# Kernel tuning notes

Measured on AMD Instinct MI355X. Metric: run time of the kernel, lower is better.

## Reference

```python
import jax, jax.numpy as jnp
import numpy as np

BS, DEC, IN_LEN, HID, EMB, VOCAB = 16, 100, 512, 768, 768, 32000


def setup_inputs() -> dict:
    key = jax.random.key(0)
    ks = jax.random.split(key, 8)
    x = jax.random.normal(ks[0], (BS, DEC, HID), dtype=jnp.float32)
    attn_dist = jax.random.normal(ks[1], (BS, DEC, IN_LEN), dtype=jnp.float32)
    enc_input = jax.random.randint(ks[2], (BS, IN_LEN), 0, VOCAB, dtype=jnp.int32)
    enc_output = jax.random.normal(ks[3], (BS, IN_LEN, EMB), dtype=jnp.float32)
    # learned params
    W_vocab = jax.random.normal(ks[4], (HID, VOCAB), dtype=jnp.float32) / np.sqrt(HID)
    b_vocab = jnp.zeros((VOCAB,), dtype=jnp.float32)
    W_gen = jax.random.normal(ks[5], (HID + EMB, 1), dtype=jnp.float32) / np.sqrt(HID + EMB)
    b_gen = jnp.zeros((1,), dtype=jnp.float32)
    return {"x": x, "attn_dist": attn_dist, "enc_input": enc_input,
            "enc_output": enc_output, "W_vocab": W_vocab, "b_vocab": b_vocab,
            "W_gen": W_gen, "b_gen": b_gen}


def reference(x, attn_dist, enc_input, enc_output, W_vocab, b_vocab, W_gen, b_gen):
    # context vector: [bs, dec, emb] = attn @ enc_output
    context = jnp.einsum('bdl,ble->bde', attn_dist, enc_output)
    mix = jnp.concatenate([context, x], axis=2)              # [bs, dec, emb+hid]
    p_gen = jax.nn.sigmoid(mix @ W_gen + b_gen)              # [bs, dec, 1]
    logit = x @ W_vocab + b_vocab                            # [bs, dec, vocab]
    vocab_dist = jax.nn.softmax(logit, axis=2) * p_gen       # [bs, dec, vocab]
    attn_w = jax.nn.softmax(attn_dist, axis=2) * (1.0 - p_gen)  # [bs, dec, in_len]
    # scatter_add attention mass onto vocab ids (duplicate ids accumulate)
    b_idx = jnp.arange(BS)[:, None, None]
    d_idx = jnp.arange(DEC)[None, :, None]
    v_idx = enc_input[:, None, :]                            # broadcast over dec
    mixed = vocab_dist.at[b_idx, d_idx, v_idx].add(attn_w)
    return jnp.log(mixed)
```

## Files before the change

### kernel.cpp

```cpp
#include <hip/hip_runtime.h>
#include <math.h>

#define BS 16
#define DEC 100
#define IN_LEN 512
#define HID 768
#define EMB 768
#define VOCAB 32000
#define NROW (BS*DEC)
#define NTILE_M 13
#define NTILE_N 250
#define KT 12
#define TILE_SHORTS 8192

using short8 = __attribute__((ext_vector_type(8))) short;
using ushort4v = __attribute__((ext_vector_type(4))) unsigned short;
using f32x4 = __attribute__((ext_vector_type(4))) float;

__device__ __forceinline__ unsigned short f2bf(float f) {
  unsigned u = __float_as_uint(f);
  u = u + 0x7FFFu + ((u >> 16) & 1u);
  return (unsigned short)(u >> 16);
}
__device__ __forceinline__ float bf2f(unsigned short h) {
  return __uint_as_float(((unsigned)h) << 16);
}

__device__ __forceinline__ void gll16(const void* g, void* l) {
  __builtin_amdgcn_global_load_lds(
      (const __attribute__((address_space(1))) unsigned int*)g,
      (__attribute__((address_space(3))) unsigned int*)l, 16, 0, 0);
}

__global__ __launch_bounds__(256) void k0_venc(const float* __restrict__ enc_out,
                                               const float* __restrict__ Wg,
                                               float* __restrict__ venc) {
  int row = blockIdx.x * 4 + (threadIdx.x >> 6);
  int lane = threadIdx.x & 63;
  const float* p = enc_out + (size_t)row * EMB;
  float s = 0.f;
  for (int e = lane; e < EMB; e += 64) s += p[e] * Wg[e];
  for (int off = 32; off; off >>= 1) s += __shfl_xor(s, off);
  if (lane == 0) venc[row] = s;
}

__global__ __launch_bounds__(256) void k1_row(const float* __restrict__ attn,
                                              const float* __restrict__ x,
                                              const float* __restrict__ venc,
                                              const float* __restrict__ Wg,
                                              const float* __restrict__ bgen,
                                              float* __restrict__ pg,
                                              float* __restrict__ lp,
                                              float* __restrict__ m_a,
                                              float* __restrict__ s_a) {
  int r = blockIdx.x;
  int b = r / DEC;
  int tid = threadIdx.x;
  const float* arow = attn + (size_t)r * IN_LEN;
  const float* ve = venc + b * IN_LEN;
  const float* xrow = x + (size_t)r * HID;

  float pdot = 0.f, m = -1e30f;
  for (int l = tid; l < IN_LEN; l += 256) { float a = arow[l]; pdot += a * ve[l]; m = fmaxf(m, a); }
  for (int h = tid; h < HID; h += 256) pdot += xrow[h] * Wg[HID + h];

  for (int off = 32; off; off >>= 1) pdot += __shfl_xor(pdot, off);
  for (int off = 32; off; off >>= 1) m = fmaxf(m, __shfl_xor(m, off));

  __shared__ float red[8];
  if ((tid & 63) == 0) { red[tid >> 6] = pdot; red[4 + (tid >> 6)] = m; }
  __syncthreads();
  float z = red[0] + red[1] + red[2] + red[3];
  m = fmaxf(fmaxf(red[4], red[5]), fmaxf(red[6], red[7]));

  float se = 0.f;
  for (int l = tid; l < IN_LEN; l += 256) se += expf(arow[l] - m);
  for (int off = 32; off; off >>= 1) se += __shfl_xor(se, off);
  __syncthreads();
  if ((tid & 63) == 0) red[tid >> 6] = se;
  __syncthreads();
  se = red[0] + red[1] + red[2] + red[3];

  if (tid == 0) {
    z += bgen[0];
    float p, l_p;
    if (z >= 0.f) { float e = expf(-z); p = 1.f / (1.f + e); l_p = -log1pf(e); }
    else          { float e = expf(z);  p = e / (1.f + e);   l_p = z - log1pf(e); }
    pg[r] = p; lp[r] = l_p; m_a[r] = m; s_a[r] = se;
  }
}

__global__ __launch_bounds__(256) void p0_pack_x(const float* __restrict__ X,
                                                 unsigned short* __restrict__ Xp) {
  int mtile = blockIdx.x, kt = blockIdx.y, tid = threadIdx.x;
  size_t base = ((size_t)(mtile * KT + kt)) * TILE_SHORTS;
#pragma unroll
  for (int i = 0; i < 4; i++) {
    int slot = tid + i * 256;
    int r = slot >> 3, s = slot & 7;
    int row = mtile * 128 + r;
    int k0 = kt * 64 + ((s ^ (r & 7)) << 3);
    short8 v;
    if (row < NROW) {
      const float* p = X + (size_t)row * HID + k0;
#pragma unroll
      for (int j = 0; j < 8; j++) v[j] = (short)f2bf(p[j]);
    } else {
#pragma unroll
      for (int j = 0; j < 8; j++) v[j] = 0;
    }
    *(short8*)&Xp[base + (size_t)slot * 8] = v;
  }
}

__global__ __launch_bounds__(256) void p0_pack_w(const float* __restrict__ W,
                                                 unsigned short* __restrict__ Wp) {
  __shared__ float ld[64][129];
  int ntile = blockIdx.x, kt = blockIdx.y, tid = threadIdx.x;
#pragma unroll
  for (int i = 0; i < 32; i++) {
    int idx = tid + i * 256;
    int kk = idx >> 7, nn = idx & 127;
    ld[kk][nn] = W[(size_t)(kt * 64 + kk) * VOCAB + ntile * 128 + nn];
  }
  __syncthreads();
  size_t base = ((size_t)(ntile * KT + kt)) * TILE_SHORTS;
#pragma unroll
  for (int i = 0; i < 4; i++) {
    int slot = tid + i * 256;
    int n = slot >> 3, s = slot & 7;
    int k0 = (s ^ (n & 7)) << 3;
    short8 v;
#pragma unroll
    for (int j = 0; j < 8; j++) v[j] = (short)f2bf(ld[k0 + j][n]);
    *(short8*)&Wp[base + (size_t)slot * 8] = v;
  }
}

__global__ __launch_bounds__(256) void k2_gemm_bf16(const unsigned short* __restrict__ Xp,
                                                    const unsigned short* __restrict__ Wp,
                                                    const float* __restrict__ bvocab,
                                                    float* __restrict__ out,
                                                    unsigned short* __restrict__ lbf,
                                                    float* __restrict__ part,
                                                    int use_bf) {
  __shared__ __align__(16) unsigned short sh[2][2][TILE_SHORTS];

  int bid = blockIdx.x;
  const int NWG = NTILE_M * NTILE_N;
  const int q = NWG / 8, rr = NWG % 8;
  int xcd = bid & 7, idx = bid >> 3;
  int wg = (xcd < rr ? xcd * (q + 1) : rr * (q + 1) + (xcd - rr) * q) + idx;
  int ntile = wg / NTILE_M, mtile = wg % NTILE_M;

  int tid = threadIdx.x;
  int wid = tid >> 6, lane = tid & 63;
  int wr = wid >> 1, wc = wid & 1;
  int l15 = lane & 15, hi = lane >> 4;

  const unsigned short* aSrc = Xp + (size_t)(mtile * KT) * TILE_SHORTS;
  const unsigned short* bSrc = Wp + (size_t)(ntile * KT) * TILE_SHORTS;

  f32x4 acc[4][4] = {};

#pragma unroll
  for (int j = 0; j < 4; j++) {
    gll16(aSrc + (size_t)(tid + j * 256) * 8, &sh[0][0][(tid + j * 256) * 8]);
    gll16(bSrc + (size_t)(tid + j * 256) * 8, &sh[0][1][(tid + j * 256) * 8]);
  }
  __syncthreads();

  int buf = 0;
  for (int kt = 0; kt < KT; kt++) {
    if (kt + 1 < KT) {
      const unsigned short* a = aSrc + (size_t)(kt + 1) * TILE_SHORTS;
      const unsigned short* b = bSrc + (size_t)(kt + 1) * TILE_SHORTS;
      int nb = buf ^ 1;
#pragma unroll
      for (int j = 0; j < 4; j++) {
        gll16(a + (size_t)(tid + j * 256) * 8, &sh[nb][0][(tid + j * 256) * 8]);
        gll16(b + (size_t)(tid + j * 256) * 8, &sh[nb][1][(tid + j * 256) * 8]);
      }
    }
    const unsigned short* A = &sh[buf][0][0];
    const unsigned short* B = &sh[buf][1][0];
#pragma unroll
    for (int ksub = 0; ksub < 2; ksub++) {
      short8 af[4], bfr[4];
#pragma unroll
      for (int mm = 0; mm < 4; mm++) {
        int r = wr * 64 + mm * 16 + l15;
        int phys = (ksub * 4 + hi) ^ (r & 7);
        af[mm] = *(const short8*)&A[r * 64 + phys * 8];
      }
#pragma unroll
      for (int nn = 0; nn < 4; nn++) {
        int n = wc * 64 + nn * 16 + l15;
        int phys = (ksub * 4 + hi) ^ (n & 7);
        bfr[nn] = *(const short8*)&B[n * 64 + phys * 8];
      }
#pragma unroll
      for (int mm = 0; mm < 4; mm++)
#pragma unroll
        for (int nn = 0; nn < 4; nn++)
          acc[mm][nn] = __builtin_amdgcn_mfma_f32_16x16x32_bf16(af[mm], bfr[nn], acc[mm][nn], 0, 0, 0);
    }
    __syncthreads();
    buf ^= 1;
  }

  float bb[4];
#pragma unroll
  for (int nn = 0; nn < 4; nn++) bb[nn] = bvocab[ntile * 128 + wc * 64 + nn * 16 + l15];
#pragma unroll
  for (int mm = 0; mm < 4; mm++)
#pragma unroll
    for (int nn = 0; nn < 4; nn++)
#pragma unroll
      for (int j = 0; j < 4; j++) acc[mm][nn][j] += bb[nn];

  float* ldsC = (float*)sh;
#pragma unroll
  for (int mm = 0; mm < 4; mm++) {
    int r0 = wr * 64 + mm * 16 + hi * 4;
#pragma unroll
    for (int nn = 0; nn < 4; nn++) {
      int c = wc * 64 + nn * 16 + l15;
#pragma unroll
      for (int j = 0; j < 4; j++) ldsC[(r0 + j) * 128 + c] = acc[mm][nn][j];
    }
  }
  __syncthreads();

  if (use_bf) {
#pragma unroll
    for (int i = 0; i < 8; i++) {
      int flat = tid + i * 256;
      int r = flat >> 4, c = (flat & 15) * 8;
      int grow = mtile * 128 + r;
      if (grow < NROW) {
        const float* p = &ldsC[r * 128 + c];
        short8 v;
#pragma unroll
        for (int j = 0; j < 8; j++) v[j] = (short)f2bf(p[j]);
        *(short8*)&lbf[(size_t)grow * VOCAB + ntile * 128 + c] = v;
      }
    }
  } else {
#pragma unroll
    for (int i = 0; i < 16; i++) {
      int flat = tid + i * 256;
      int r = flat >> 5, c = (flat & 31) * 4;
      int grow = mtile * 128 + r;
      if (grow < NROW)
        *(float4*)&out[(size_t)grow * VOCAB + ntile * 128 + c] = *(const float4*)&ldsC[r * 128 + c];
    }
  }
  __syncthreads();

  float* red = (float*)sh;
#pragma unroll
  for (int mm = 0; mm < 4; mm++) {
#pragma unroll
    for (int j = 0; j < 4; j++) {
      float mx = fmaxf(fmaxf(acc[mm][0][j], acc[mm][1][j]),
                       fmaxf(acc[mm][2][j], acc[mm][3][j]));
      mx = fmaxf(mx, __shfl_xor(mx, 1));
      mx = fmaxf(mx, __shfl_xor(mx, 2));
      mx = fmaxf(mx, __shfl_xor(mx, 4));
      mx = fmaxf(mx, __shfl_xor(mx, 8));
      float sl = __expf(acc[mm][0][j] - mx) + __expf(acc[mm][1][j] - mx) +
                 __expf(acc[mm][2][j] - mx) + __expf(acc[mm][3][j] - mx);
      sl += __shfl_xor(sl, 1);
      sl += __shfl_xor(sl, 2);
      sl += __shfl_xor(sl, 4);
      sl += __shfl_xor(sl, 8);
      if (l15 == 0) {
        int rloc = wr * 64 + mm * 16 + hi * 4 + j;
        int o = (rloc * 2 + wc) * 2;
        red[o] = mx; red[o + 1] = sl;
      }
    }
  }
  __syncthreads();
  if (tid < 128) {
    int o0 = (tid * 2 + 0) * 2;
    int o1 = (tid * 2 + 1) * 2;
    float m0 = red[o0], s0 = red[o0 + 1];
    float m1 = red[o1], s1 = red[o1 + 1];
    float m = fmaxf(m0, m1);
    float s = s0 * __expf(m0 - m) + s1 * __expf(m1 - m);
    int grow = mtile * 128 + tid;
    if (grow < NROW) {
      part[(size_t)grow * 500 + ntile * 2]     = m;
      part[(size_t)grow * 500 + ntile * 2 + 1] = s;
    }
  }
}

__global__ __launch_bounds__(256) void k4_finish(float* __restrict__ out,
                                                 const float* __restrict__ part,
                                                 const float* __restrict__ lp) {
  int r = blockIdx.x >> 1, half = blockIdx.x & 1;
  int tid = threadIdx.x;
  float m = -1e30f, s = 0.f;
  if (tid < NTILE_N) {
    m = part[(size_t)r * 500 + tid * 2];
    s = part[(size_t)r * 500 + tid * 2 + 1];
  }
  for (int off = 1; off < 64; off <<= 1) {
    float mo = __shfl_xor(m, off), so = __shfl_xor(s, off);
    float nm = fmaxf(m, mo);
    s = s * __expf(m - nm) + so * __expf(mo - nm);
    m = nm;
  }
  __shared__ float sm[4], ss[4], sc[1];
  if ((tid & 63) == 0) { sm[tid >> 6] = m; ss[tid >> 6] = s; }
  __syncthreads();
  if (tid == 0) {
    float mm_ = sm[0], ss_ = ss[0];
    for (int w = 1; w < 4; w++) {
      float nm = fmaxf(mm_, sm[w]);
      ss_ = ss_ * __expf(mm_ - nm) + ss[w] * __expf(sm[w] - nm);
      mm_ = nm;
    }
    sc[0] = lp[r] - (mm_ + __logf(ss_));
  }
  __syncthreads();
  float coef = sc[0];
  float4* p = (float4*)(out + (size_t)r * VOCAB + half * (VOCAB / 2));
  for (int i = tid; i < VOCAB / 8; i += 256) {
    float4 v = p[i];
    v.x += coef; v.y += coef; v.z += coef; v.w += coef;
    p[i] = v;
  }
}

__global__ __launch_bounds__(256) void k4_finish_bf(float* __restrict__ out,
                                                    const unsigned short* __restrict__ lbf,
                                                    const float* __restrict__ part,
                                                    const float* __restrict__ lp) {
  int r = blockIdx.x;
  int tid = threadIdx.x;
  float m = -1e30f, s = 0.f;
  if (tid < NTILE_N) {
    m = part[(size_t)r * 500 + tid * 2];
    s = part[(size_t)r * 500 + tid * 2 + 1];
  }
  for (int off = 1; off < 64; off <<= 1) {
    float mo = __shfl_xor(m, off), so = __shfl_xor(s, off);
    float nm = fmaxf(m, mo);
    s = s * __expf(m - nm) + so * __expf(mo - nm);
    m = nm;
  }
  __shared__ float sm[4], ss[4], sc[1];
  if ((tid & 63) == 0) { sm[tid >> 6] = m; ss[tid >> 6] = s; }
  __syncthreads();
  if (tid == 0) {
    float mm_ = sm[0], ss_ = ss[0];
    for (int w = 1; w < 4; w++) {
      float nm = fmaxf(mm_, sm[w]);
      ss_ = ss_ * __expf(mm_ - nm) + ss[w] * __expf(sm[w] - nm);
      mm_ = nm;
    }
    sc[0] = lp[r] - (mm_ + __logf(ss_));
  }
  __syncthreads();
  float coef = sc[0];
  const short8* src = (const short8*)(lbf + (size_t)r * VOCAB);
  float* dst = out + (size_t)r * VOCAB;
  for (int i = tid; i < VOCAB / 8; i += 256) {
    short8 v = src[i];
    float4 a, b;
    a.x = bf2f((unsigned short)v[0]) + coef; a.y = bf2f((unsigned short)v[1]) + coef;
    a.z = bf2f((unsigned short)v[2]) + coef; a.w = bf2f((unsigned short)v[3]) + coef;
    b.x = bf2f((unsigned short)v[4]) + coef; b.y = bf2f((unsigned short)v[5]) + coef;
    b.z = bf2f((unsigned short)v[6]) + coef; b.w = bf2f((unsigned short)v[7]) + coef;
    *(float4*)&dst[i * 8]     = a;
    *(float4*)&dst[i * 8 + 4] = b;
  }
}

__global__ __launch_bounds__(256) void k4_scatter(float* __restrict__ out,
                                                  const float* __restrict__ attn,
                                                  const int* __restrict__ enc,
                                                  const float* __restrict__ pg,
                                                  const float* __restrict__ m_a,
                                                  const float* __restrict__ s_a) {
  int idx = blockIdx.x * 256 + threadIdx.x;
  int l = idx & (IN_LEN - 1);
  int r = idx >> 9;
  int b = r / DEC;
  float omp = 1.f - pg[r];
  if (omp <= 0.f) return;
  float term = omp * expf(attn[(size_t)r * IN_LEN + l] - m_a[r]) / s_a[r];
  int v = enc[b * IN_LEN + l];
  unsigned* ua = (unsigned*)(out + (size_t)r * VOCAB + v);
  unsigned old = *ua;
  while (true) {
    float f = __uint_as_float(old);
    float nf = logf(expf(f) + term);
    unsigned assumed = old;
    old = atomicCAS(ua, assumed, __float_as_uint(nf));
    if (old == assumed) break;
  }
}

#define BM 128
#define BN 128
#define BK 32
__device__ __forceinline__ int swz_old(int row, int k) {
  int slot = (k >> 3) ^ ((row >> 1) & 3);
  return row * 32 + slot * 8 + (k & 7);
}

__global__ __launch_bounds__(256) void k2_gemm_old(const float* __restrict__ X,
                                                   const float* __restrict__ W,
                                                   const float* __restrict__ bvocab,
                                                   float* __restrict__ out) {
  __shared__ __align__(16) unsigned short As[BM * BK];
  __shared__ __align__(16) unsigned short Bs[BN * BK];
  const int mtile = blockIdx.x;
  const int ntile = blockIdx.y;
  const int tid = threadIdx.x;
  const int wid = tid >> 6, lane = tid & 63;
  const int wr = wid >> 1, wc = wid & 1;
  f32x4 acc[4][4] = {};
  float4 areg[4];
  float  breg[16];
  const int nl = tid & 127;
  const int kg = tid >> 7;
  {
#pragma unroll
    for (int i = 0; i < 4; i++) {
      int idx = tid + i * 256;
      int r = mtile * BM + (idx >> 3);
      if (r < NROW) areg[i] = *(const float4*)(X + (size_t)r * HID + (idx & 7) * 4);
      else areg[i] = make_float4(0.f, 0.f, 0.f, 0.f);
    }
    const float* base = W + (size_t)(kg * 16) * VOCAB + ntile * BN + nl;
#pragma unroll
    for (int i = 0; i < 16; i++) breg[i] = base[(size_t)i * VOCAB];
  }
  const int KS = HID / BK;
  for (int ks = 0; ks < KS; ++ks) {
#pragma unroll
    for (int i = 0; i < 4; i++) {
      int idx = tid + i * 256;
      int r = idx >> 3, kq = idx & 7;
      ushort4v w;
      w[0] = f2bf(areg[i].x); w[1] = f2bf(areg[i].y);
      w[2] = f2bf(areg[i].z); w[3] = f2bf(areg[i].w);
      *(ushort4v*)&As[swz_old(r, kq * 4)] = w;
    }
    {
      short8 v0, v1;
#pragma unroll
      for (int i = 0; i < 8; i++) { v0[i] = (short)f2bf(breg[i]); v1[i] = (short)f2bf(breg[8 + i]); }
      *(short8*)&Bs[swz_old(nl, kg * 16)] = v0;
      *(short8*)&Bs[swz_old(nl, kg * 16 + 8)] = v1;
    }
    __syncthreads();
    if (ks + 1 < KS) {
      const int ksn = ks + 1;
#pragma unroll
      for (int i = 0; i < 4; i++) {
        int idx = tid + i * 256;
        int r = mtile * BM + (idx >> 3);
        if (r < NROW) areg[i] = *(const float4*)(X + (size_t)r * HID + ksn * BK + (idx & 7) * 4);
        else areg[i] = make_float4(0.f, 0.f, 0.f, 0.f);
      }
      const float* base = W + (size_t)(ksn * BK + kg * 16) * VOCAB + ntile * BN + nl;
#pragma unroll
      for (int i = 0; i < 16; i++) breg[i] = base[(size_t)i * VOCAB];
    }
    {
      const int k0 = (lane >> 4) * 8;
      const int rbase = wr * 64 + (lane & 15);
      const int cbase = wc * 64 + (lane & 15);
      short8 af[4], bf[4];
#pragma unroll
      for (int mm = 0; mm < 4; mm++) af[mm] = *(const short8*)&As[swz_old(rbase + mm * 16, k0)];
#pragma unroll
      for (int nn = 0; nn < 4; nn++) bf[nn] = *(const short8*)&Bs[swz_old(cbase + nn * 16, k0)];
#pragma unroll
      for (int mm = 0; mm < 4; mm++)
#pragma unroll
        for (int nn = 0; nn < 4; nn++)
          acc[mm][nn] = __builtin_amdgcn_mfma_f32_16x16x32_bf16(af[mm], bf[nn], acc[mm][nn], 0, 0, 0);
    }
    __syncthreads();
  }
#pragma unroll
  for (int mm = 0; mm < 4; mm++) {
    int row0 = mtile * BM + wr * 64 + mm * 16 + (lane >> 4) * 4;
#pragma unroll
    for (int nn = 0; nn < 4; nn++) {
      int col = ntile * BN + wc * 64 + nn * 16 + (lane & 15);
      float bb = bvocab[col];
#pragma unroll
      for (int j = 0; j < 4; j++) {
        int row = row0 + j;
        if (row < NROW) out[(size_t)row * VOCAB + col] = acc[mm][nn][j] + bb;
      }
    }
  }
}

__global__ __launch_bounds__(256) void k3_norm(float* __restrict__ out,
                                               const float* __restrict__ lp) {
  int r = blockIdx.x;
  float4* row = reinterpret_cast<float4*>(out + (size_t)r * VOCAB);
  int tid = threadIdx.x;
  float m = -1e30f, s = 0.f;
  for (int i = tid; i < VOCAB / 4; i += 256) {
    float4 v = row[i];
    float m4 = fmaxf(fmaxf(v.x, v.y), fmaxf(v.z, v.w));
    if (m4 > m) { s *= __expf(m - m4); m = m4; }
    s += __expf(v.x - m) + __expf(v.y - m) + __expf(v.z - m) + __expf(v.w - m);
  }
  for (int off = 32; off; off >>= 1) {
    float mo = __shfl_xor(m, off), so = __shfl_xor(s, off);
    float nm = fmaxf(m, mo);
    s = s * __expf(m - nm) + so * __expf(mo - nm);
    m = nm;
  }
  __shared__ float mred[4], sred[4];
  if ((tid & 63) == 0) { mred[tid >> 6] = m; sred[tid >> 6] = s; }
  __syncthreads();
  if (tid == 0) {
    float mm = mred[0], ss = sred[0];
    for (int w = 1; w < 4; w++) {
      float mo = mred[w], so = sred[w];
      float nm = fmaxf(mm, mo);
      ss = ss * __expf(mm - nm) + so * __expf(mo - nm);
      mm = nm;
    }
    mred[0] = mm; sred[0] = ss;
  }
  __syncthreads();
  m = mred[0]; s = sred[0];
  float coef = lp[r] - (m + __logf(s));
  for (int i = tid; i < VOCAB / 4; i += 256) {
    float4 v = row[i];
    v.x += coef; v.y += coef; v.z += coef; v.w += coef;
    row[i] = v;
  }
}

extern "C" void kernel_launch(void* const* d_in, const int* in_sizes, int n_in,
                              void* d_out, int out_size, void* d_ws, size_t ws_size,
                              hipStream_t stream) {
  (void)in_sizes; (void)n_in; (void)out_size;
  const float* x       = (const float*)d_in[0];
  const float* attn    = (const float*)d_in[1];
  const int*   enc_in  = (const int*)d_in[2];
  const float* enc_out = (const float*)d_in[3];
  const float* Wv      = (const float*)d_in[4];
  const float* bv      = (const float*)d_in[5];
  const float* Wg      = (const float*)d_in[6];
  const float* bg      = (const float*)d_in[7];
  float* out = (float*)d_out;
  float* ws  = (float*)d_ws;

  float* venc = ws;
  float* pg   = ws + 8192;
  float* lp   = ws + 9792;
  float* m_a  = ws + 11392;
  float* s_a  = ws + 12992;
  float* part = ws + 14592;
  unsigned short* Xp = (unsigned short*)(ws + 814592);
  unsigned short* Wp = (unsigned short*)(ws + 1453568);
  unsigned short* Lbf = (unsigned short*)(ws + 13741568);
  const size_t NEED  = (size_t)13741568 * 4;
  const size_t NEED2 = NEED + (size_t)NROW * VOCAB * 2;

  hipLaunchKernelGGL(k0_venc, dim3(2048), dim3(256), 0, stream, enc_out, Wg, venc);
  hipLaunchKernelGGL(k1_row, dim3(NROW), dim3(256), 0, stream, attn, x, venc, Wg, bg,
                     pg, lp, m_a, s_a);

  if (ws_size >= NEED) {
    int use_bf = (ws_size >= NEED2) ? 1 : 0;
    hipLaunchKernelGGL(p0_pack_x, dim3(NTILE_M, KT), dim3(256), 0, stream, x, Xp);
    hipLaunchKernelGGL(p0_pack_w, dim3(NTILE_N, KT), dim3(256), 0, stream, Wv, Wp);
    hipLaunchKernelGGL(k2_gemm_bf16, dim3(NTILE_M * NTILE_N), dim3(256), 0, stream,
                       Xp, Wp, bv, out, Lbf, part, use_bf);
    if (use_bf) {
      hipLaunchKernelGGL(k4_finish_bf, dim3(NROW), dim3(256), 0, stream, out, Lbf, part, lp);
    } else {
      hipLaunchKernelGGL(k4_finish, dim3(NROW * 2), dim3(256), 0, stream, out, part, lp);
    }
    hipLaunchKernelGGL(k4_scatter, dim3((NROW * IN_LEN) / 256), dim3(256), 0, stream,
                       out, attn, enc_in, pg, m_a, s_a);
  } else {
    hipLaunchKernelGGL(k2_gemm_old, dim3(NTILE_M, NTILE_N), dim3(256), 0, stream,
                       x, Wv, bv, out);
    hipLaunchKernelGGL(k3_norm, dim3(NROW), dim3(256), 0, stream, out, lp);
    hipLaunchKernelGGL(k4_scatter, dim3((NROW * IN_LEN) / 256), dim3(256), 0, stream,
                       out, attn, enc_in, pg, m_a, s_a);
  }
}
```

Measured before the change: 293.8 us.

## Widen GEMM tile to 128x256 with triple-buffered K32 pipeline and bf16 LDS epilogue

The vocab GEMM now uses 128x256 output tiles and K-steps of 32 instead of 128x128 and 64. It loads through a three-stage LDS ring with explicit vmcnt waits so two stages of loads are in flight, and raises MFMA priority with setprio. The epilogue writes bf16 values into LDS and copies them out with wide stores, and the partial softmax stats are resized. The finish kernel uses 512 threads. The aim is more reuse of each A/B tile, fewer workgroups and better overlap of loads with compute, at the cost of more accumulator registers (32 f32x4) and possible occupancy limits.

```diff
diff --git a/kernel.cpp b/kernel.cpp
--- a/kernel.cpp
+++ b/kernel.cpp
@@ -9,9 +9,10 @@
 #define VOCAB 32000
 #define NROW (BS*DEC)
 #define NTILE_M 13
-#define NTILE_N 250
-#define KT 12
-#define TILE_SHORTS 8192
+#define NTILE_N2 125
+#define KT2 24
+#define A_SHORTS 4096
+#define B_SHORTS 8192
 
 using short8 = __attribute__((ext_vector_type(8))) short;
 using ushort4v = __attribute__((ext_vector_type(4))) unsigned short;
@@ -92,14 +93,14 @@
 
 __global__ __launch_bounds__(256) void p0_pack_x(const float* __restrict__ X,
                                                  unsigned short* __restrict__ Xp) {
-  int mtile = blockIdx.x, kt = blockIdx.y, tid = threadIdx.x;
-  size_t base = ((size_t)(mtile * KT + kt)) * TILE_SHORTS;
-#pragma unroll
-  for (int i = 0; i < 4; i++) {
+  int mtile = blockIdx.x, ks = blockIdx.y, tid = threadIdx.x;
+  size_t base = ((size_t)(mtile * KT2 + ks)) * A_SHORTS;
+#pragma unroll
+  for (int i = 0; i < 2; i++) {
     int slot = tid + i * 256;
-    int r = slot >> 3, s = slot & 7;
+    int r = slot >> 2, s = slot & 3;
     int row = mtile * 128 + r;
-    int k0 = kt * 64 + ((s ^ (r & 7)) << 3);
+    int k0 = ks * 32 + ((s ^ (r & 3)) << 3);
     short8 v;
     if (row < NROW) {
       const float* p = X + (size_t)row * HID + k0;
@@ -115,21 +116,21 @@
 
 __global__ __launch_bounds__(256) void p0_pack_w(const float* __restrict__ W,
                                                  unsigned short* __restrict__ Wp) {
-  __shared__ float ld[64][129];
-  int ntile = blockIdx.x, kt = blockIdx.y, tid = threadIdx.x;
+  __shared__ float ld[32][257];
+  int ntile = blockIdx.x, ks = blockIdx.y, tid = threadIdx.x;
 #pragma unroll
   for (int i = 0; i < 32; i++) {
     int idx = tid + i * 256;
-    int kk = idx >> 7, nn = idx & 127;
-    ld[kk][nn] = W[(size_t)(kt * 64 + kk) * VOCAB + ntile * 128 + nn];
-  }
-  __syncthreads();
-  size_t base = ((size_t)(ntile * KT + kt)) * TILE_SHORTS;
+    int kk = idx >> 8, nn = idx & 255;
+    ld[kk][nn] = W[(size_t)(ks * 32 + kk) * VOCAB + ntile * 256 + nn];
+  }
+  __syncthreads();
+  size_t base = ((size_t)(ntile * KT2 + ks)) * B_SHORTS;
 #pragma unroll
   for (int i = 0; i < 4; i++) {
     int slot = tid + i * 256;
-    int n = slot >> 3, s = slot & 7;
-    int k0 = (s ^ (n & 7)) << 3;
+    int n = slot >> 2, s = slot & 3;
+    int k0 = (s ^ (n & 3)) << 3;
     short8 v;
 #pragma unroll
     for (int j = 0; j < 8; j++) v[j] = (short)f2bf(ld[k0 + j][n]);
@@ -137,140 +138,143 @@
   }
 }
 
-__global__ __launch_bounds__(256) void k2_gemm_bf16(const unsigned short* __restrict__ Xp,
-                                                    const unsigned short* __restrict__ Wp,
-                                                    const float* __restrict__ bvocab,
-                                                    float* __restrict__ out,
-                                                    unsigned short* __restrict__ lbf,
-                                                    float* __restrict__ part,
-                                                    int use_bf) {
-  __shared__ __align__(16) unsigned short sh[2][2][TILE_SHORTS];
+__global__ __launch_bounds__(256, 2) void k2_gemm_v4(const unsigned short* __restrict__ Xp,
+                                                     const unsigned short* __restrict__ Wp,
+                                                     const float* __restrict__ bvocab,
+                                                     float* __restrict__ out,
+                                                     unsigned short* __restrict__ lbf,
+                                                     float* __restrict__ part,
+                                                     int use_bf) {
+  __shared__ __align__(16) unsigned short sh[3][12288];
 
   int bid = blockIdx.x;
-  const int NWG = NTILE_M * NTILE_N;
+  const int NWG = NTILE_M * NTILE_N2;
   const int q = NWG / 8, rr = NWG % 8;
   int xcd = bid & 7, idx = bid >> 3;
   int wg = (xcd < rr ? xcd * (q + 1) : rr * (q + 1) + (xcd - rr) * q) + idx;
   int ntile = wg / NTILE_M, mtile = wg % NTILE_M;
 
-  int tid = threadIdx.x;
-  int wid = tid >> 6, lane = tid & 63;
-  int wr = wid >> 1, wc = wid & 1;
-  int l15 = lane & 15, hi = lane >> 4;
-
-  const unsigned short* aSrc = Xp + (size_t)(mtile * KT) * TILE_SHORTS;
-  const unsigned short* bSrc = Wp + (size_t)(ntile * KT) * TILE_SHORTS;
-
-  f32x4 acc[4][4] = {};
-
-#pragma unroll
-  for (int j = 0; j < 4; j++) {
-    gll16(aSrc + (size_t)(tid + j * 256) * 8, &sh[0][0][(tid + j * 256) * 8]);
-    gll16(bSrc + (size_t)(tid + j * 256) * 8, &sh[0][1][(tid + j * 256) * 8]);
-  }
-  __syncthreads();
-
-  int buf = 0;
-  for (int kt = 0; kt < KT; kt++) {
-    if (kt + 1 < KT) {
-      const unsigned short* a = aSrc + (size_t)(kt + 1) * TILE_SHORTS;
-      const unsigned short* b = bSrc + (size_t)(kt + 1) * TILE_SHORTS;
-      int nb = buf ^ 1;
-#pragma unroll
-      for (int j = 0; j < 4; j++) {
-        gll16(a + (size_t)(tid + j * 256) * 8, &sh[nb][0][(tid + j * 256) * 8]);
-        gll16(b + (size_t)(tid + j * 256) * 8, &sh[nb][1][(tid + j * 256) * 8]);
+  const int tid = threadIdx.x;
+  const int wid = tid >> 6, lane = tid & 63;
+  const int wr = wid >> 1, wc = wid & 1;
+  const int l15 = lane & 15, hi = lane >> 4;
+  const int phys = (hi ^ (l15 & 3)) * 8;
+
+  const unsigned short* aSrc = Xp + (size_t)(mtile * KT2) * A_SHORTS;
+  const unsigned short* bSrc = Wp + (size_t)(ntile * KT2) * B_SHORTS;
+
+  const int aoff = (wr * 64 + l15) * 32 + phys;
+  const int boff = (wc * 128 + l15) * 32 + phys;
+
+  f32x4 acc[4][8] = {};
+
+#pragma unroll
+  for (int t = 0; t < 2; t++) {
+    const unsigned short* a = aSrc + (size_t)t * A_SHORTS;
+    const unsigned short* b = bSrc + (size_t)t * B_SHORTS;
+    unsigned short* dA = &sh[t][0];
+    unsigned short* dB = &sh[t][4096];
+    gll16(a + (size_t)tid * 8,            dA + tid * 8);
+    gll16(a + (size_t)(tid + 256) * 8,    dA + (tid + 256) * 8);
+#pragma unroll
+    for (int j2 = 0; j2 < 4; j2++)
+      gll16(b + (size_t)(tid + j2 * 256) * 8, dB + (tid + j2 * 256) * 8);
+  }
+  asm volatile("s_waitcnt vmcnt(6)" ::: "memory");
+  __builtin_amdgcn_s_barrier();
+  asm volatile("" ::: "memory");
+
+  int bcur = 0;
+  for (int t = 0; t < KT2; ++t) {
+    if (t + 2 < KT2) {
+      int bn = bcur + 2; if (bn >= 3) bn -= 3;
+      const unsigned short* a = aSrc + (size_t)(t + 2) * A_SHORTS;
+      const unsigned short* b = bSrc + (size_t)(t + 2) * B_SHORTS;
+      unsigned short* dA = &sh[bn][0];
+      unsigned short* dB = &sh[bn][4096];
+      gll16(a + (size_t)tid * 8,            dA + tid * 8);
+      gll16(a + (size_t)(tid + 256) * 8,    dA + (tid + 256) * 8);
+#pragma unroll
+      for (int j2 = 0; j2 < 4; j2++)
+        gll16(b + (size_t)(tid + j2 * 256) * 8, dB + (tid + j2 * 256) * 8);
+    }
+    const unsigned short* A = &sh[bcur][0];
+    const unsigned short* B = &sh[bcur][4096];
+    short8 af[4], bfr[8];
+#pragma unroll
+    for (int mm = 0; mm < 4; mm++) af[mm] = *(const short8*)&A[aoff + mm * 512];
+#pragma unroll
+    for (int nn = 0; nn < 8; nn++) bfr[nn] = *(const short8*)&B[boff + nn * 512];
+    __builtin_amdgcn_s_setprio(1);
+#pragma unroll
+    for (int mm = 0; mm < 4; mm++)
+#pragma unroll
+      for (int nn = 0; nn < 8; nn++)
+        acc[mm][nn] = __builtin_amdgcn_mfma_f32_16x16x32_bf16(af[mm], bfr[nn], acc[mm][nn], 0, 0, 0);
+    __builtin_amdgcn_s_setprio(0);
+    if (t < KT2 - 2) { asm volatile("s_waitcnt vmcnt(6)" ::: "memory"); }
+    else             { asm volatile("s_waitcnt vmcnt(0)" ::: "memory"); }
+    __builtin_amdgcn_s_barrier();
+    asm volatile("" ::: "memory");
+    bcur = bcur + 1; if (bcur >= 3) bcur = 0;
+  }
+
+  __syncthreads();
+
+  float bb[8];
+#pragma unroll
+  for (int nn = 0; nn < 8; nn++) bb[nn] = bvocab[ntile * 256 + wc * 128 + nn * 16 + l15];
+#pragma unroll
+  for (int mm = 0; mm < 4; mm++)
+#pragma unroll
+    for (int nn = 0; nn < 8; nn++)
+#pragma unroll
+      for (int j = 0; j < 4; j++) acc[mm][nn][j] += bb[nn];
+
+  unsigned short* ldsC = &sh[0][0];
+  float* red = (float*)&sh[2][8192];
+
+  if (use_bf) {
+#pragma unroll
+    for (int mm = 0; mm < 4; mm++) {
+      int row0 = wr * 64 + mm * 16 + hi * 4;
+#pragma unroll
+      for (int nn = 0; nn < 8; nn++) {
+        int col = wc * 128 + nn * 16 + l15;
+#pragma unroll
+        for (int j = 0; j < 4; j++) ldsC[(row0 + j) * 256 + col] = f2bf(acc[mm][nn][j]);
       }
     }
-    const unsigned short* A = &sh[buf][0][0];
-    const unsigned short* B = &sh[buf][1][0];
-#pragma unroll
-    for (int ksub = 0; ksub < 2; ksub++) {
-      short8 af[4], bfr[4];
-#pragma unroll
-      for (int mm = 0; mm < 4; mm++) {
-        int r = wr * 64 + mm * 16 + l15;
-        int phys = (ksub * 4 + hi) ^ (r & 7);
-        af[mm] = *(const short8*)&A[r * 64 + phys * 8];
+  } else {
+#pragma unroll
+    for (int mm = 0; mm < 4; mm++) {
+      int row0 = mtile * 128 + wr * 64 + mm * 16 + hi * 4;
+#pragma unroll
+      for (int nn = 0; nn < 8; nn++) {
+        int col = ntile * 256 + wc * 128 + nn * 16 + l15;
+#pragma unroll
+        for (int j = 0; j < 4; j++) {
+          int row = row0 + j;
+          if (row < NROW) out[(size_t)row * VOCAB + col] = acc[mm][nn][j];
+        }
       }
-#pragma unroll
-      for (int nn = 0; nn < 4; nn++) {
-        int n = wc * 64 + nn * 16 + l15;
-        int phys = (ksub * 4 + hi) ^ (n & 7);
-        bfr[nn] = *(const short8*)&B[n * 64 + phys * 8];
-      }
-#pragma unroll
-      for (int mm = 0; mm < 4; mm++)
-#pragma unroll
-        for (int nn = 0; nn < 4; nn++)
-          acc[mm][nn] = __builtin_amdgcn_mfma_f32_16x16x32_bf16(af[mm], bfr[nn], acc[mm][nn], 0, 0, 0);
-    }
-    __syncthreads();
-    buf ^= 1;
-  }
-
-  float bb[4];
-#pragma unroll
-  for (int nn = 0; nn < 4; nn++) bb[nn] = bvocab[ntile * 128 + wc * 64 + nn * 16 + l15];
-#pragma unroll
-  for (int mm = 0; mm < 4; mm++)
-#pragma unroll
-    for (int nn = 0; nn < 4; nn++)
-#pragma unroll
-      for (int j = 0; j < 4; j++) acc[mm][nn][j] += bb[nn];
-
-  float* ldsC = (float*)sh;
+    }
+  }
+
 #pragma unroll
   for (int mm = 0; mm < 4; mm++) {
-    int r0 = wr * 64 + mm * 16 + hi * 4;
-#pragma unroll
-    for (int nn = 0; nn < 4; nn++) {
-      int c = wc * 64 + nn * 16 + l15;
-#pragma unroll
-      for (int j = 0; j < 4; j++) ldsC[(r0 + j) * 128 + c] = acc[mm][nn][j];
-    }
-  }
-  __syncthreads();
-
-  if (use_bf) {
-#pragma unroll
-    for (int i = 0; i < 8; i++) {
-      int flat = tid + i * 256;
-      int r = flat >> 4, c = (flat & 15) * 8;
-      int grow = mtile * 128 + r;
-      if (grow < NROW) {
-        const float* p = &ldsC[r * 128 + c];
-        short8 v;
-#pragma unroll
-        for (int j = 0; j < 8; j++) v[j] = (short)f2bf(p[j]);
-        *(short8*)&lbf[(size_t)grow * VOCAB + ntile * 128 + c] = v;
-      }
-    }
-  } else {
-#pragma unroll
-    for (int i = 0; i < 16; i++) {
-      int flat = tid + i * 256;
-      int r = flat >> 5, c = (flat & 31) * 4;
-      int grow = mtile * 128 + r;
-      if (grow < NROW)
-        *(float4*)&out[(size_t)grow * VOCAB + ntile * 128 + c] = *(const float4*)&ldsC[r * 128 + c];
-    }
-  }
-  __syncthreads();
-
-  float* red = (float*)sh;
-#pragma unroll
-  for (int mm = 0; mm < 4; mm++) {
 #pragma unroll
     for (int j = 0; j < 4; j++) {
-      float mx = fmaxf(fmaxf(acc[mm][0][j], acc[mm][1][j]),
-                       fmaxf(acc[mm][2][j], acc[mm][3][j]));
+      float mx = acc[mm][0][j];
+#pragma unroll
+      for (int nn = 1; nn < 8; nn++) mx = fmaxf(mx, acc[mm][nn][j]);
       mx = fmaxf(mx, __shfl_xor(mx, 1));
       mx = fmaxf(mx, __shfl_xor(mx, 2));
       mx = fmaxf(mx, __shfl_xor(mx, 4));
       mx = fmaxf(mx, __shfl_xor(mx, 8));
-      float sl = __expf(acc[mm][0][j] - mx) + __expf(acc[mm][1][j] - mx) +
-                 __expf(acc[mm][2][j] - mx) + __expf(acc[mm][3][j] - mx);
+      float sl = 0.f;
+#pragma unroll
+      for (int nn = 0; nn < 8; nn++) sl += __expf(acc[mm][nn][j] - mx);
       sl += __shfl_xor(sl, 1);
       sl += __shfl_xor(sl, 2);
       sl += __shfl_xor(sl, 4);
@@ -283,6 +287,17 @@
     }
   }
   __syncthreads();
+
+  if (use_bf) {
+#pragma unroll
+    for (int i = 0; i < 16; i++) {
+      int flat = tid + i * 256;
+      int r = flat >> 5, c = (flat & 31) * 8;
+      int grow = mtile * 128 + r;
+      if (grow < NROW)
+        *(short8*)&lbf[(size_t)grow * VOCAB + ntile * 256 + c] = *(const short8*)&ldsC[r * 256 + c];
+    }
+  }
   if (tid < 128) {
     int o0 = (tid * 2 + 0) * 2;
     int o1 = (tid * 2 + 1) * 2;
@@ -292,60 +307,22 @@
     float s = s0 * __expf(m0 - m) + s1 * __expf(m1 - m);
     int grow = mtile * 128 + tid;
     if (grow < NROW) {
-      part[(size_t)grow * 500 + ntile * 2]     = m;
-      part[(size_t)grow * 500 + ntile * 2 + 1] = s;
-    }
-  }
-}
-
-__global__ __launch_bounds__(256) void k4_finish(float* __restrict__ out,
-                                                 const float* __restrict__ part,
-                                                 const float* __restrict__ lp) {
-  int r = blockIdx.x >> 1, half = blockIdx.x & 1;
-  int tid = threadIdx.x;
-  float m = -1e30f, s = 0.f;
-  if (tid < NTILE_N) {
-    m = part[(size_t)r * 500 + tid * 2];
-    s = part[(size_t)r * 500 + tid * 2 + 1];
-  }
-  for (int off = 1; off < 64; off <<= 1) {
-    float mo = __shfl_xor(m, off), so = __shfl_xor(s, off);
-    float nm = fmaxf(m, mo);
-    s = s * __expf(m - nm) + so * __expf(mo - nm);
-    m = nm;
-  }
-  __shared__ float sm[4], ss[4], sc[1];
-  if ((tid & 63) == 0) { sm[tid >> 6] = m; ss[tid >> 6] = s; }
-  __syncthreads();
-  if (tid == 0) {
-    float mm_ = sm[0], ss_ = ss[0];
-    for (int w = 1; w < 4; w++) {
-      float nm = fmaxf(mm_, sm[w]);
-      ss_ = ss_ * __expf(mm_ - nm) + ss[w] * __expf(sm[w] - nm);
-      mm_ = nm;
-    }
-    sc[0] = lp[r] - (mm_ + __logf(ss_));
-  }
-  __syncthreads();
-  float coef = sc[0];
-  float4* p = (float4*)(out + (size_t)r * VOCAB + half * (VOCAB / 2));
-  for (int i = tid; i < VOCAB / 8; i += 256) {
-    float4 v = p[i];
-    v.x += coef; v.y += coef; v.z += coef; v.w += coef;
-    p[i] = v;
-  }
-}
-
-__global__ __launch_bounds__(256) void k4_finish_bf(float* __restrict__ out,
+      part[(size_t)grow * 256 + ntile * 2]     = m;
+      part[(size_t)grow * 256 + ntile * 2 + 1] = s;
+    }
+  }
+}
+
+__global__ __launch_bounds__(512) void k4_finish_bf(float* __restrict__ out,
                                                     const unsigned short* __restrict__ lbf,
                                                     const float* __restrict__ part,
                                                     const float* __restrict__ lp) {
   int r = blockIdx.x;
   int tid = threadIdx.x;
   float m = -1e30f, s = 0.f;
-  if (tid < NTILE_N) {
-    m = part[(size_t)r * 500 + tid * 2];
-    s = part[(size_t)r * 500 + tid * 2 + 1];
+  if (tid < NTILE_N2) {
+    m = part[(size_t)r * 256 + tid * 2];
+    s = part[(size_t)r * 256 + tid * 2 + 1];
   }
   for (int off = 1; off < 64; off <<= 1) {
     float mo = __shfl_xor(m, off), so = __shfl_xor(s, off);
@@ -353,12 +330,12 @@
     s = s * __expf(m - nm) + so * __expf(mo - nm);
     m = nm;
   }
-  __shared__ float sm[4], ss[4], sc[1];
+  __shared__ float sm[8], ss[8], sc[1];
   if ((tid & 63) == 0) { sm[tid >> 6] = m; ss[tid >> 6] = s; }
   __syncthreads();
   if (tid == 0) {
     float mm_ = sm[0], ss_ = ss[0];
-    for (int w = 1; w < 4; w++) {
+    for (int w = 1; w < 8; w++) {
       float nm = fmaxf(mm_, sm[w]);
       ss_ = ss_ * __expf(mm_ - nm) + ss[w] * __expf(sm[w] - nm);
       mm_ = nm;
@@ -369,7 +346,7 @@
   float coef = sc[0];
   const short8* src = (const short8*)(lbf + (size_t)r * VOCAB);
   float* dst = out + (size_t)r * VOCAB;
-  for (int i = tid; i < VOCAB / 8; i += 256) {
+  for (int i = tid; i < VOCAB / 8; i += 512) {
     short8 v = src[i];
     float4 a, b;
     a.x = bf2f((unsigned short)v[0]) + coef; a.y = bf2f((unsigned short)v[1]) + coef;
@@ -378,6 +355,44 @@
     b.z = bf2f((unsigned short)v[6]) + coef; b.w = bf2f((unsigned short)v[7]) + coef;
     *(float4*)&dst[i * 8]     = a;
     *(float4*)&dst[i * 8 + 4] = b;
+  }
+}
+
+__global__ __launch_bounds__(256) void k4_finish(float* __restrict__ out,
+                                                 const float* __restrict__ part,
+                                                 const float* __restrict__ lp) {
+  int r = blockIdx.x >> 1, half = blockIdx.x & 1;
+  int tid = threadIdx.x;
+  float m = -1e30f, s = 0.f;
+  if (tid < NTILE_N2) {
+    m = part[(size_t)r * 256 + tid * 2];
+    s = part[(size_t)r * 256 + tid * 2 + 1];
+  }
+  for (int off = 1; off < 64; off <<= 1) {
+    float mo = __shfl_xor(m, off), so = __shfl_xor(s, off);
+    float nm = fmaxf(m, mo);
+    s = s * __expf(m - nm) + so * __expf(mo - nm);
+    m = nm;
+  }
+  __shared__ float sm[4], ss[4], sc[1];
+  if ((tid & 63) == 0) { sm[tid >> 6] = m; ss[tid >> 6] = s; }
+  __syncthreads();
+  if (tid == 0) {
+    float mm_ = sm[0], ss_ = ss[0];
+    for (int w = 1; w < 4; w++) {
+      float nm = fmaxf(mm_, sm[w]);
+      ss_ = ss_ * __expf(mm_ - nm) + ss[w] * __expf(sm[w] - nm);
+      mm_ = nm;
+    }
+    sc[0] = lp[r] - (mm_ + __logf(ss_));
+  }
+  __syncthreads();
+  float coef = sc[0];
+  float4* p = (float4*)(out + (size_t)r * VOCAB + half * (VOCAB / 2));
+  for (int i = tid; i < VOCAB / 8; i += 256) {
+    float4 v = p[i];
+    v.x += coef; v.y += coef; v.z += coef; v.w += coef;
+    p[i] = v;
   }
 }
 
@@ -581,19 +596,19 @@
 
   if (ws_size >= NEED) {
     int use_bf = (ws_size >= NEED2) ? 1 : 0;
-    hipLaunchKernelGGL(p0_pack_x, dim3(NTILE_M, KT), dim3(256), 0, stream, x, Xp);
-    hipLaunchKernelGGL(p0_pack_w, dim3(NTILE_N, KT), dim3(256), 0, stream, Wv, Wp);
-    hipLaunchKernelGGL(k2_gemm_bf16, dim3(NTILE_M * NTILE_N), dim3(256), 0, stream,
+    hipLaunchKernelGGL(p0_pack_x, dim3(NTILE_M, KT2), dim3(256), 0, stream, x, Xp);
+    hipLaunchKernelGGL(p0_pack_w, dim3(NTILE_N2, KT2), dim3(256), 0, stream, Wv, Wp);
+    hipLaunchKernelGGL(k2_gemm_v4, dim3(NTILE_M * NTILE_N2), dim3(256), 0, stream,
                        Xp, Wp, bv, out, Lbf, part, use_bf);
     if (use_bf) {
-      hipLaunchKernelGGL(k4_finish_bf, dim3(NROW), dim3(256), 0, stream, out, Lbf, part, lp);
+      hipLaunchKernelGGL(k4_finish_bf, dim3(NROW), dim3(512), 0, stream, out, Lbf, part, lp);
     } else {
       hipLaunchKernelGGL(k4_finish, dim3(NROW * 2), dim3(256), 0, stream, out, part, lp);
     }
     hipLaunchKernelGGL(k4_scatter, dim3((NROW * IN_LEN) / 256), dim3(256), 0, stream,
                        out, attn, enc_in, pg, m_a, s_a);
   } else {
-    hipLaunchKernelGGL(k2_gemm_old, dim3(NTILE_M, NTILE_N), dim3(256), 0, stream,
+    hipLaunchKernelGGL(k2_gemm_old, dim3(NTILE_M, 250), dim3(256), 0, stream,
                        x, Wv, bv, out);
     hipLaunchKernelGGL(k3_norm, dim3(NROW), dim3(256), 0, stream, out, lp);
     hipLaunchKernelGGL(k4_scatter, dim3((NROW * IN_LEN) / 256), dim3(256), 0, stream,
```

New measurement: 276.8 us. -5.8%, faster.

## Fuse scatter into finish kernel with LDS hash; single-buffer GEMM LDS staging

Applied to the files above, without the earlier changes.

Merges the log-softmax finish pass and the attention scatter into one per-row kernel. It aggregates duplicate vocab ids in an LDS hash table and then applies log(exp(p)+sum) to the touched entries, which removes a separate kernel and its global atomics. The GEMM drops LDS double buffering so each K step loads and then syncs, which halves LDS use but serialises loads with compute. Its epilogue writes bf16 directly into LDS, and the fp32 path stores straight from registers. The fused update goes through exp and log again, which adds rounding error.

```diff
diff --git a/kernel.cpp b/kernel.cpp
--- a/kernel.cpp
+++ b/kernel.cpp
@@ -11,7 +11,7 @@
 #define NTILE_M 13
 #define NTILE_N 250
 #define KT 12
-#define TILE_SHORTS 8192
+#define T_SHORTS 8192
 
 using short8 = __attribute__((ext_vector_type(8))) short;
 using ushort4v = __attribute__((ext_vector_type(4))) unsigned short;
@@ -93,7 +93,7 @@
 __global__ __launch_bounds__(256) void p0_pack_x(const float* __restrict__ X,
                                                  unsigned short* __restrict__ Xp) {
   int mtile = blockIdx.x, kt = blockIdx.y, tid = threadIdx.x;
-  size_t base = ((size_t)(mtile * KT + kt)) * TILE_SHORTS;
+  size_t base = ((size_t)(mtile * KT + kt)) * T_SHORTS;
 #pragma unroll
   for (int i = 0; i < 4; i++) {
     int slot = tid + i * 256;
@@ -124,7 +124,7 @@
     ld[kk][nn] = W[(size_t)(kt * 64 + kk) * VOCAB + ntile * 128 + nn];
   }
   __syncthreads();
-  size_t base = ((size_t)(ntile * KT + kt)) * TILE_SHORTS;
+  size_t base = ((size_t)(ntile * KT + kt)) * T_SHORTS;
 #pragma unroll
   for (int i = 0; i < 4; i++) {
     int slot = tid + i * 256;
@@ -137,14 +137,15 @@
   }
 }
 
-__global__ __launch_bounds__(256) void k2_gemm_bf16(const unsigned short* __restrict__ Xp,
-                                                    const unsigned short* __restrict__ Wp,
-                                                    const float* __restrict__ bvocab,
-                                                    float* __restrict__ out,
-                                                    unsigned short* __restrict__ lbf,
-                                                    float* __restrict__ part,
-                                                    int use_bf) {
-  __shared__ __align__(16) unsigned short sh[2][2][TILE_SHORTS];
+__global__ __launch_bounds__(256) void k2_gemm_v5(const unsigned short* __restrict__ Xp,
+                                                  const unsigned short* __restrict__ Wp,
+                                                  const float* __restrict__ bvocab,
+                                                  float* __restrict__ out,
+                                                  unsigned short* __restrict__ lbf,
+                                                  float* __restrict__ part,
+                                                  int use_bf) {
+  __shared__ __align__(16) unsigned short sh[2 * T_SHORTS];
+  __shared__ float red[512];
 
   int bid = blockIdx.x;
   const int NWG = NTILE_M * NTILE_N;
@@ -153,37 +154,28 @@
   int wg = (xcd < rr ? xcd * (q + 1) : rr * (q + 1) + (xcd - rr) * q) + idx;
   int ntile = wg / NTILE_M, mtile = wg % NTILE_M;
 
-  int tid = threadIdx.x;
-  int wid = tid >> 6, lane = tid & 63;
-  int wr = wid >> 1, wc = wid & 1;
-  int l15 = lane & 15, hi = lane >> 4;
-
-  const unsigned short* aSrc = Xp + (size_t)(mtile * KT) * TILE_SHORTS;
-  const unsigned short* bSrc = Wp + (size_t)(ntile * KT) * TILE_SHORTS;
+  const int tid = threadIdx.x;
+  const int wid = tid >> 6, lane = tid & 63;
+  const int wr = wid >> 1, wc = wid & 1;
+  const int l15 = lane & 15, hi = lane >> 4;
+
+  const unsigned short* aSrc = Xp + (size_t)(mtile * KT) * T_SHORTS;
+  const unsigned short* bSrc = Wp + (size_t)(ntile * KT) * T_SHORTS;
+  unsigned short* shA = &sh[0];
+  unsigned short* shB = &sh[T_SHORTS];
 
   f32x4 acc[4][4] = {};
 
-#pragma unroll
-  for (int j = 0; j < 4; j++) {
-    gll16(aSrc + (size_t)(tid + j * 256) * 8, &sh[0][0][(tid + j * 256) * 8]);
-    gll16(bSrc + (size_t)(tid + j * 256) * 8, &sh[0][1][(tid + j * 256) * 8]);
-  }
-  __syncthreads();
-
-  int buf = 0;
-  for (int kt = 0; kt < KT; kt++) {
-    if (kt + 1 < KT) {
-      const unsigned short* a = aSrc + (size_t)(kt + 1) * TILE_SHORTS;
-      const unsigned short* b = bSrc + (size_t)(kt + 1) * TILE_SHORTS;
-      int nb = buf ^ 1;
-#pragma unroll
-      for (int j = 0; j < 4; j++) {
-        gll16(a + (size_t)(tid + j * 256) * 8, &sh[nb][0][(tid + j * 256) * 8]);
-        gll16(b + (size_t)(tid + j * 256) * 8, &sh[nb][1][(tid + j * 256) * 8]);
-      }
-    }
-    const unsigned short* A = &sh[buf][0][0];
-    const unsigned short* B = &sh[buf][1][0];
+  for (int kt = 0; kt < KT; ++kt) {
+    const unsigned short* a = aSrc + (size_t)kt * T_SHORTS;
+    const unsigned short* b = bSrc + (size_t)kt * T_SHORTS;
+#pragma unroll
+    for (int p = 0; p < 4; p++) {
+      gll16(a + (size_t)(tid + p * 256) * 8, shA + (tid + p * 256) * 8);
+      gll16(b + (size_t)(tid + p * 256) * 8, shB + (tid + p * 256) * 8);
+    }
+    __syncthreads();
+
 #pragma unroll
     for (int ksub = 0; ksub < 2; ksub++) {
       short8 af[4], bfr[4];
@@ -191,13 +183,13 @@
       for (int mm = 0; mm < 4; mm++) {
         int r = wr * 64 + mm * 16 + l15;
         int phys = (ksub * 4 + hi) ^ (r & 7);
-        af[mm] = *(const short8*)&A[r * 64 + phys * 8];
+        af[mm] = *(const short8*)&shA[r * 64 + phys * 8];
       }
 #pragma unroll
       for (int nn = 0; nn < 4; nn++) {
         int n = wc * 64 + nn * 16 + l15;
         int phys = (ksub * 4 + hi) ^ (n & 7);
-        bfr[nn] = *(const short8*)&B[n * 64 + phys * 8];
+        bfr[nn] = *(const short8*)&shB[n * 64 + phys * 8];
       }
 #pragma unroll
       for (int mm = 0; mm < 4; mm++)
@@ -206,7 +198,6 @@
           acc[mm][nn] = __builtin_amdgcn_mfma_f32_16x16x32_bf16(af[mm], bfr[nn], acc[mm][nn], 0, 0, 0);
     }
     __syncthreads();
-    buf ^= 1;
   }
 
   float bb[4];
@@ -219,46 +210,35 @@
 #pragma unroll
       for (int j = 0; j < 4; j++) acc[mm][nn][j] += bb[nn];
 
-  float* ldsC = (float*)sh;
-#pragma unroll
-  for (int mm = 0; mm < 4; mm++) {
-    int r0 = wr * 64 + mm * 16 + hi * 4;
-#pragma unroll
-    for (int nn = 0; nn < 4; nn++) {
-      int c = wc * 64 + nn * 16 + l15;
-#pragma unroll
-      for (int j = 0; j < 4; j++) ldsC[(r0 + j) * 128 + c] = acc[mm][nn][j];
-    }
-  }
-  __syncthreads();
+  unsigned short* ldsC = &sh[0];
 
   if (use_bf) {
 #pragma unroll
-    for (int i = 0; i < 8; i++) {
-      int flat = tid + i * 256;
-      int r = flat >> 4, c = (flat & 15) * 8;
-      int grow = mtile * 128 + r;
-      if (grow < NROW) {
-        const float* p = &ldsC[r * 128 + c];
-        short8 v;
-#pragma unroll
-        for (int j = 0; j < 8; j++) v[j] = (short)f2bf(p[j]);
-        *(short8*)&lbf[(size_t)grow * VOCAB + ntile * 128 + c] = v;
+    for (int mm = 0; mm < 4; mm++) {
+      int row0 = wr * 64 + mm * 16 + hi * 4;
+#pragma unroll
+      for (int nn = 0; nn < 4; nn++) {
+        int col = wc * 64 + nn * 16 + l15;
+#pragma unroll
+        for (int j = 0; j < 4; j++) ldsC[(row0 + j) * 128 + col] = f2bf(acc[mm][nn][j]);
       }
     }
   } else {
 #pragma unroll
-    for (int i = 0; i < 16; i++) {
-      int flat = tid + i * 256;
-      int r = flat >> 5, c = (flat & 31) * 4;
-      int grow = mtile * 128 + r;
-      if (grow < NROW)
-        *(float4*)&out[(size_t)grow * VOCAB + ntile * 128 + c] = *(const float4*)&ldsC[r * 128 + c];
-    }
-  }
-  __syncthreads();
-
-  float* red = (float*)sh;
+    for (int mm = 0; mm < 4; mm++) {
+      int row0 = mtile * 128 + wr * 64 + mm * 16 + hi * 4;
+#pragma unroll
+      for (int nn = 0; nn < 4; nn++) {
+        int col = ntile * 128 + wc * 64 + nn * 16 + l15;
+#pragma unroll
+        for (int j = 0; j < 4; j++) {
+          int row = row0 + j;
+          if (row < NROW) out[(size_t)row * VOCAB + col] = acc[mm][nn][j];
+        }
+      }
+    }
+  }
+
 #pragma unroll
   for (int mm = 0; mm < 4; mm++) {
 #pragma unroll
@@ -283,6 +263,17 @@
     }
   }
   __syncthreads();
+
+  if (use_bf) {
+#pragma unroll
+    for (int i = 0; i < 8; i++) {
+      int flat = tid + i * 256;
+      int r = flat >> 4, c = (flat & 15) * 8;
+      int grow = mtile * 128 + r;
+      if (grow < NROW)
+        *(short8*)&lbf[(size_t)grow * VOCAB + ntile * 128 + c] = *(const short8*)&ldsC[r * 128 + c];
+    }
+  }
   if (tid < 128) {
     int o0 = (tid * 2 + 0) * 2;
     int o1 = (tid * 2 + 1) * 2;
@@ -298,6 +289,85 @@
   }
 }
 
+__global__ __launch_bounds__(512) void k4_fused(float* __restrict__ out,
+                                                const unsigned short* __restrict__ lbf,
+                                                const float* __restrict__ part,
+                                                const float* __restrict__ lp,
+                                                const float* __restrict__ attn,
+                                                const int* __restrict__ enc,
+                                                const float* __restrict__ pg,
+                                                const float* __restrict__ m_a,
+                                                const float* __restrict__ s_a) {
+  int r = blockIdx.x;
+  int tid = threadIdx.x;
+  __shared__ float sm[8], ss[8], sc[1];
+  __shared__ int   s_key[1024];
+  __shared__ float s_val[1024];
+  s_key[tid] = -1; s_key[tid + 512] = -1;
+  s_val[tid] = 0.f; s_val[tid + 512] = 0.f;
+
+  float m = -1e30f, s = 0.f;
+  if (tid < NTILE_N) {
+    m = part[(size_t)r * 500 + tid * 2];
+    s = part[(size_t)r * 500 + tid * 2 + 1];
+  }
+  for (int off = 1; off < 64; off <<= 1) {
+    float mo = __shfl_xor(m, off), so = __shfl_xor(s, off);
+    float nm = fmaxf(m, mo);
+    s = s * __expf(m - nm) + so * __expf(mo - nm);
+    m = nm;
+  }
+  if ((tid & 63) == 0) { sm[tid >> 6] = m; ss[tid >> 6] = s; }
+  __syncthreads();
+  if (tid == 0) {
+    float mm_ = sm[0], ss_ = ss[0];
+    for (int w = 1; w < 8; w++) {
+      float nm = fmaxf(mm_, sm[w]);
+      ss_ = ss_ * __expf(mm_ - nm) + ss[w] * __expf(sm[w] - nm);
+      mm_ = nm;
+    }
+    sc[0] = lp[r] - (mm_ + __logf(ss_));
+  }
+
+  float omp = 1.f - pg[r];
+  if (omp > 0.f) {
+    int b_ = r / DEC;
+    float t = omp * __expf(attn[(size_t)r * IN_LEN + tid] - m_a[r]) / s_a[r];
+    int v = enc[b_ * IN_LEN + tid];
+    int slot = v & 1023;
+    while (true) {
+      int old = atomicCAS(&s_key[slot], -1, v);
+      if (old == -1 || old == v) { atomicAdd(&s_val[slot], t); break; }
+      slot = (slot + 1) & 1023;
+    }
+  }
+  __syncthreads();
+  float coef = sc[0];
+
+  const short8* src = (const short8*)(lbf + (size_t)r * VOCAB);
+  float* dst = out + (size_t)r * VOCAB;
+  for (int i = tid; i < VOCAB / 8; i += 512) {
+    short8 v = src[i];
+    float4 a, b;
+    a.x = bf2f((unsigned short)v[0]) + coef; a.y = bf2f((unsigned short)v[1]) + coef;
+    a.z = bf2f((unsigned short)v[2]) + coef; a.w = bf2f((unsigned short)v[3]) + coef;
+    b.x = bf2f((unsigned short)v[4]) + coef; b.y = bf2f((unsigned short)v[5]) + coef;
+    b.z = bf2f((unsigned short)v[6]) + coef; b.w = bf2f((unsigned short)v[7]) + coef;
+    *(float4*)&dst[i * 8]     = a;
+    *(float4*)&dst[i * 8 + 4] = b;
+  }
+  __syncthreads();
+
+  for (int i = tid; i < 1024; i += 512) {
+    int v = s_key[i];
+    if (v >= 0) {
+      float sum = s_val[i];
+      float p = dst[v];
+      dst[v] = logf(expf(p) + sum);
+    }
+  }
+}
+
 __global__ __launch_bounds__(256) void k4_finish(float* __restrict__ out,
                                                  const float* __restrict__ part,
                                                  const float* __restrict__ lp) {
@@ -333,51 +403,6 @@
     float4 v = p[i];
     v.x += coef; v.y += coef; v.z += coef; v.w += coef;
     p[i] = v;
-  }
-}
-
-__global__ __launch_bounds__(256) void k4_finish_bf(float* __restrict__ out,
-                                                    const unsigned short* __restrict__ lbf,
-                                                    const float* __restrict__ part,
-                                                    const float* __restrict__ lp) {
-  int r = blockIdx.x;
-  int tid = threadIdx.x;
-  float m = -1e30f, s = 0.f;
-  if (tid < NTILE_N) {
-    m = part[(size_t)r * 500 + tid * 2];
-    s = part[(size_t)r * 500 + tid * 2 + 1];
-  }
-  for (int off = 1; off < 64; off <<= 1) {
-    float mo = __shfl_xor(m, off), so = __shfl_xor(s, off);
-    float nm = fmaxf(m, mo);
-    s = s * __expf(m - nm) + so * __expf(mo - nm);
-    m = nm;
-  }
-  __shared__ float sm[4], ss[4], sc[1];
-  if ((tid & 63) == 0) { sm[tid >> 6] = m; ss[tid >> 6] = s; }
-  __syncthreads();
-  if (tid == 0) {
-    float mm_ = sm[0], ss_ = ss[0];
-    for (int w = 1; w < 4; w++) {
-      float nm = fmaxf(mm_, sm[w]);
-      ss_ = ss_ * __expf(mm_ - nm) + ss[w] * __expf(sm[w] - nm);
-      mm_ = nm;
-    }
-    sc[0] = lp[r] - (mm_ + __logf(ss_));
-  }
-  __syncthreads();
-  float coef = sc[0];
-  const short8* src = (const short8*)(lbf + (size_t)r * VOCAB);
-  float* dst = out + (size_t)r * VOCAB;
-  for (int i = tid; i < VOCAB / 8; i += 256) {
-    short8 v = src[i];
-    float4 a, b;
-    a.x = bf2f((unsigned short)v[0]) + coef; a.y = bf2f((unsigned short)v[1]) + coef;
-    a.z = bf2f((unsigned short)v[2]) + coef; a.w = bf2f((unsigned short)v[3]) + coef;
-    b.x = bf2f((unsigned short)v[4]) + coef; b.y = bf2f((unsigned short)v[5]) + coef;
-    b.z = bf2f((unsigned short)v[6]) + coef; b.w = bf2f((unsigned short)v[7]) + coef;
-    *(float4*)&dst[i * 8]     = a;
-    *(float4*)&dst[i * 8 + 4] = b;
   }
 }
 
@@ -583,17 +608,18 @@
     int use_bf = (ws_size >= NEED2) ? 1 : 0;
     hipLaunchKernelGGL(p0_pack_x, dim3(NTILE_M, KT), dim3(256), 0, stream, x, Xp);
     hipLaunchKernelGGL(p0_pack_w, dim3(NTILE_N, KT), dim3(256), 0, stream, Wv, Wp);
-    hipLaunchKernelGGL(k2_gemm_bf16, dim3(NTILE_M * NTILE_N), dim3(256), 0, stream,
+    hipLaunchKernelGGL(k2_gemm_v5, dim3(NTILE_M * NTILE_N), dim3(256), 0, stream,
                        Xp, Wp, bv, out, Lbf, part, use_bf);
     if (use_bf) {
-      hipLaunchKernelGGL(k4_finish_bf, dim3(NROW), dim3(256), 0, stream, out, Lbf, part, lp);
+      hipLaunchKernelGGL(k4_fused, dim3(NROW), dim3(512), 0, stream,
+                         out, Lbf, part, lp, attn, enc_in, pg, m_a, s_a);
     } else {
       hipLaunchKernelGGL(k4_finish, dim3(NROW * 2), dim3(256), 0, stream, out, part, lp);
-    }
-    hipLaunchKernelGGL(k4_scatter, dim3((NROW * IN_LEN) / 256), dim3(256), 0, stream,
-                       out, attn, enc_in, pg, m_a, s_a);
+      hipLaunchKernelGGL(k4_scatter, dim3((NROW * IN_LEN) / 256), dim3(256), 0, stream,
+                         out, attn, enc_in, pg, m_a, s_a);
+    }
   } else {
-    hipLaunchKernelGGL(k2_gemm_old, dim3(NTILE_M, NTILE_N), dim3(256), 0, stream,
+    hipLaunchKernelGGL(k2_gemm_old, dim3(NTILE_M, 250), dim3(256), 0, stream,
                        x, Wv, bv, out);
     hipLaunchKernelGGL(k3_norm, dim3(NROW), dim3(256), 0, stream, out, lp);
     hipLaunchKernelGGL(k4_scatter, dim3((NROW * IN_LEN) / 256), dim3(256), 0, stream,
```

Result: faster. 275.6 us (-6.2%).
